# Optimization experiments

Hardware: AMD Instinct MI355X
Metric: run time of the kernel (lower is better)

Reference implementation:

```python
import jax, jax.numpy as jnp
import numpy as np

BS, L, K, SIM, CIN, COUT, HID = 8, 256, 5, 4, 32, 32, 64
LEXP = (SIM + 1) * (L - 1) + 1  # 1276


def setup_inputs() -> dict:
    key = jax.random.key(0)
    ks = jax.random.split(key, 6)
    # event timestamps: sorted within each sequence
    true_times = jnp.sort(jax.random.uniform(ks[0], (BS, L)) * 100.0, axis=-1)
    times = jnp.sort(jax.random.uniform(ks[1], (BS, LEXP)) * 100.0, axis=-1)
    true_features = jax.random.normal(ks[2], (BS, L, CIN))
    non_pad_mask = jnp.ones((BS, L), dtype=bool)
    # per-pair kernel MLP: (..., CIN) -> (..., CIN, COUT)
    W1 = jax.random.normal(ks[3], (CIN, HID)) * 0.1
    b1 = jnp.zeros((HID,))
    W2 = jax.random.normal(ks[4], (HID, CIN * COUT)) * 0.1
    b2 = jnp.zeros((CIN * COUT,))
    return dict(times=times, true_times=true_times, true_features=true_features,
                non_pad_mask=non_pad_mask, W1=W1, b1=b1, W2=W2, b2=b2, sim_size=SIM)


def _temporal_enc(dt, cin):
    # sin on even channels, cos on odd channels of dt / 10000^(2*(i//2)/cin)
    pos = jnp.asarray([10000.0 ** (2.0 * (i // 2) / cin) for i in range(cin)], dt.dtype)
    r = dt[..., None] / pos
    parity = jnp.arange(cin) % 2
    return jnp.where(parity == 0, jnp.sin(r), jnp.cos(r))


def reference(times, true_times, true_features, non_pad_mask, W1, b1, W2, b2, sim_size):
    bs, Lm = true_times.shape
    cin = true_features.shape[-1]
    # The torch identity-conv1d trick gathers, per output position t, the
    # kernel_size events at lags K..1 (t+j-K, j=0..K-1), zero-padded on the left.
    idx = jnp.arange(Lm)[None, :] + jnp.arange(K)[:, None]          # (K, L) indices into left-padded seq
    tt_pad = jnp.pad(true_times, ((0, 0), (K, 0)))
    pct = tt_pad[:, idx]                                            # (bs, K, L)
    tf_pad = jnp.pad(true_features, ((0, 0), (K, 0), (0, 0)))
    pcf = tf_pad[:, idx, :]                                         # (bs, K, L, cin)
    m_pad = jnp.pad(non_pad_mask, ((0, 0), (K, 0)))
    dt_mask = m_pad[:, idx] & non_pad_mask[:, None, :]              # (bs, K, L)

    s = int(sim_size)
    rep = s + 1
    # expand each true-time slot over the sim grid: Lexp = rep*(L-1)+1
    pct = jnp.repeat(pct, rep, axis=-1)
    pcf = jnp.repeat(pcf, rep, axis=2)
    dtm = jnp.repeat(dt_mask, rep, axis=-1)
    if s > 0:
        pct = pct[..., :-s]
        pcf = pcf[:, :, :-s, :]
    dtm = dtm[..., s:]                                              # mask shifted by sim_size (as in torch)

    delta = times[:, None, :] - pct                                 # (bs, K, Lexp)
    delta = jnp.where(dtm, delta, 0.0)
    pcf = jnp.where(dtm[..., None], pcf, 0.0)

    te = _temporal_enc(delta, cin)                                  # (bs, K, Lexp, cin)
    h = jax.nn.relu(te @ W1 + b1)
    kv = (h @ W2 + b2).reshape(*te.shape[:-1], cin, W2.shape[-1] // cin)  # (bs,K,Lexp,cin,cout)
    # torch also zeroes kv at ~dt_mask, but pcf is already zero there, so the
    # product (and its gradients) are identical without the redundant mask.
    out = jnp.einsum('bkli,bklio->blo', pcf, kv)                    # sum over K and cin
    return out
```

## Files before the change

### kernel.cpp

```cpp
#include <hip/hip_runtime.h>
#include <hip/hip_bf16.h>
#include <math.h>

#define BS   8
#define LL   256
#define KK   5
#define REP  5
#define LEXP 1276
#define TPB  40
#define NTILE (BS*TPB)
#define NF   12

typedef __attribute__((ext_vector_type(8)))  short bf16x8;
typedef __attribute__((ext_vector_type(16))) float f32x16;
typedef __attribute__((ext_vector_type(4)))  int   int4v;

__device__ __forceinline__ int pk_bf16(float lo, float hi) {
  __hip_bfloat162 v = __float22bfloat162_rn(make_float2(lo, hi));
  union { __hip_bfloat162 b; int i; } u; u.b = v; return u.i;
}
__device__ __forceinline__ bf16x8 to_bf(int4v v) {
  union { int4v i; bf16x8 b; } u; u.i = v; return u.b;
}

__device__ __constant__ const float IPC_TAB[16] = {
  0.15915494309189535f,   0.08950250709812862f,  0.050331651737107575f, 0.028302732511355427f,
  0.015915494309189534f,  0.008950250709812862f, 0.005033165173710758f, 0.002830273251135543f,
  0.0015915494309189536f, 0.0008950250709812862f,0.0005033165173710758f,0.0002830273251135543f,
  0.00015915494309189535f,8.950250709812862e-05f,5.033165173710758e-05f,2.830273251135543e-05f
};

__global__ __launch_bounds__(256) void k_w2f(
    const float* __restrict__ W2,
    int4v* __restrict__ W2F)
{
  const int u = blockIdx.x * 256 + threadIdx.x;
  const int nt = u >> 7, s = (u >> 6) & 1, lane = u & 63;
  const int col = lane & 31, hi = lane >> 5;
  const int np = nt * 32 + col, o = np >> 6, h = np & 63;
  const float* w2p = W2 + h * 1024 + o;
  int4v v;
  #pragma unroll
  for (int d = 0; d < 4; ++d) {
    const int i = s * 16 + hi * 8 + 2 * d;
    v[d] = pk_bf16(w2p[i * 32], w2p[(i + 1) * 32]);
  }
  W2F[u] = v;
}

__global__ __launch_bounds__(512) void k_fused(
    const float* __restrict__ times,
    const float* __restrict__ TT,
    const float* __restrict__ tf,
    const float* __restrict__ W1,
    const float* __restrict__ b1,
    const float* __restrict__ b2,
    const int4v* __restrict__ W2F,
    float* __restrict__ out)
{
  __shared__ unsigned short Al[NF][2048];
  __shared__ float Bcs[NF][32];

  const int t    = threadIdx.x;
  const int w    = t >> 6, lane = t & 63;
  const int col  = lane & 31, hi = lane >> 5;

  const int tile = blockIdx.x;
  const int b    = tile / TPB;
  const int j0   = (tile - b * TPB) * 32;
  const int jq_lo = j0 / REP;
  const int jtop  = (j0 + 31 < LEXP) ? (j0 + 31) : (LEXP - 1);
  const int jq_hi = jtop / REP;
  const int f_lo  = (jq_lo >= KK) ? (jq_lo - KK) : 0;
  const int f_hi  = jq_hi - 1;
  const int nf    = f_hi - f_lo + 1;

  bf16x8 tff[2];
  {
    const bool vf = col < nf;
    const float* tfp = tf + (size_t)(b * LL + f_lo + (vf ? col : 0)) * 32;
    #pragma unroll
    for (int s = 0; s < 2; ++s) {
      int4v v;
      #pragma unroll
      for (int d = 0; d < 4; ++d) {
        const int i = s * 16 + hi * 8 + 2 * d;
        v[d] = vf ? pk_bf16(tfp[i], tfp[i + 1]) : 0;
      }
      tff[s] = to_bf(v);
    }
  }

  #pragma unroll 2
  for (int nt = w; nt < 64; nt += 8) {
    const int4v a0 = W2F[(nt * 2 + 0) * 64 + lane];
    const int4v a1 = W2F[(nt * 2 + 1) * 64 + lane];
    f32x16 c = {};
    c = __builtin_amdgcn_mfma_f32_32x32x16_bf16(to_bf(a0), tff[0], c, 0, 0, 0);
    c = __builtin_amdgcn_mfma_f32_32x32x16_bf16(to_bf(a1), tff[1], c, 0, 0, 0);
    if (col < nf) {
      #pragma unroll
      for (int q = 0; q < 4; ++q) {
        const int u  = nt * 4 + q;
        const int up = u ^ ((u >> 3) & 7) ^ (col & 7);
        uint2 d2;
        d2.x = (unsigned)pk_bf16(c[4*q+0], c[4*q+1]);
        d2.y = (unsigned)pk_bf16(c[4*q+2], c[4*q+3]);
        *(uint2*)((char*)&Al[0][0] + col * 4096 + up * 16 + hi * 8) = d2;
      }
    }
  }

  if (t < NF * 32) {
    const int fl = t >> 5, o = t & 31;
    if (fl < nf) {
      const float* tfp = tf + (size_t)(b * LL + f_lo + fl) * 32;
      float acc = 0.0f;
      #pragma unroll
      for (int i = 0; i < 32; ++i) acc += tfp[i] * b2[i * 32 + o];
      Bcs[fl][o] = acc;
    }
  }

  int4v w1f[2][2];
  #pragma unroll
  for (int t2 = 0; t2 < 2; ++t2)
    #pragma unroll
    for (int ks = 0; ks < 2; ++ks) {
      const int h = t2 * 32 + col, c0 = ks * 16 + hi * 8;
      int4v v;
      v.x = pk_bf16(W1[(c0 + 0) * 64 + h], W1[(c0 + 1) * 64 + h]);
      v.y = pk_bf16(W1[(c0 + 2) * 64 + h], W1[(c0 + 3) * 64 + h]);
      v.z = pk_bf16(W1[(c0 + 4) * 64 + h], W1[(c0 + 5) * 64 + h]);
      v.w = pk_bf16(W1[(c0 + 6) * 64 + h], W1[(c0 + 7) * 64 + h]);
      w1f[t2][ks] = v;
    }
  f32x16 b1c0 = {}, b1c1 = {};
  #pragma unroll
  for (int gg = 0; gg < 16; ++gg) {
    const int rh = (gg & 3) + 8 * (gg >> 2) + 4 * hi;
    b1c0[gg] = b1[rh]; b1c1[gg] = b1[32 + rh];
  }
  float ipc[2][4];
  #pragma unroll
  for (int ks = 0; ks < 2; ++ks)
    #pragma unroll
    for (int d = 0; d < 4; ++d)
      ipc[ks][d] = IPC_TAB[hi * 4 + ks * 8 + d];

  const int j   = j0 + col;
  const bool vj = j < LEXP;
  const int jq  = (vj ? j : LEXP - 1) / REP;
  const float tj = times[b * LEXP + (vj ? j : LEXP - 1)];

  __syncthreads();

  f32x16 co = {};
  for (int fl = w; fl < nf; fl += 8) {
    const int f = f_lo + fl;
    int4v af[4];
    #pragma unroll
    for (int s = 0; s < 4; ++s) {
      const int u  = col * 8 + s * 2 + hi;
      const int up = u ^ ((u >> 3) & 7) ^ (fl & 7);
      af[s] = *(const int4v*)((const char*)&Al[0][0] + fl * 4096 + up * 16);
    }
    const float dt = tj - TT[b * LL + f];
    const int dd   = jq - f;
    const bool vm  = vj && (dd >= 1) && (dd <= KK);

    int4v te0, te1;
    {
      float r;
      r = dt * ipc[0][0]; te0.x = vm ? pk_bf16(__builtin_amdgcn_sinf(r), __builtin_amdgcn_cosf(r)) : 0;
      r = dt * ipc[0][1]; te0.y = vm ? pk_bf16(__builtin_amdgcn_sinf(r), __builtin_amdgcn_cosf(r)) : 0;
      r = dt * ipc[0][2]; te0.z = vm ? pk_bf16(__builtin_amdgcn_sinf(r), __builtin_amdgcn_cosf(r)) : 0;
      r = dt * ipc[0][3]; te0.w = vm ? pk_bf16(__builtin_amdgcn_sinf(r), __builtin_amdgcn_cosf(r)) : 0;
      r = dt * ipc[1][0]; te1.x = vm ? pk_bf16(__builtin_amdgcn_sinf(r), __builtin_amdgcn_cosf(r)) : 0;
      r = dt * ipc[1][1]; te1.y = vm ? pk_bf16(__builtin_amdgcn_sinf(r), __builtin_amdgcn_cosf(r)) : 0;
      r = dt * ipc[1][2]; te1.z = vm ? pk_bf16(__builtin_amdgcn_sinf(r), __builtin_amdgcn_cosf(r)) : 0;
      r = dt * ipc[1][3]; te1.w = vm ? pk_bf16(__builtin_amdgcn_sinf(r), __builtin_amdgcn_cosf(r)) : 0;
    }

    f32x16 h0 = __builtin_amdgcn_mfma_f32_32x32x16_bf16(to_bf(w1f[0][0]), to_bf(te0), b1c0, 0, 0, 0);
    h0 = __builtin_amdgcn_mfma_f32_32x32x16_bf16(to_bf(w1f[0][1]), to_bf(te1), h0, 0, 0, 0);
    f32x16 h1 = __builtin_amdgcn_mfma_f32_32x32x16_bf16(to_bf(w1f[1][0]), to_bf(te0), b1c1, 0, 0, 0);
    h1 = __builtin_amdgcn_mfma_f32_32x32x16_bf16(to_bf(w1f[1][1]), to_bf(te1), h1, 0, 0, 0);
    #pragma unroll
    for (int gg = 0; gg < 16; ++gg) { h0[gg] = fmaxf(h0[gg], 0.0f); h1[gg] = fmaxf(h1[gg], 0.0f); }

    #pragma unroll
    for (int s = 0; s < 4; ++s) {
      const int off = (s & 1) * 8;
      float e0,e1,e2,e3,e4,e5,e6,e7;
      if (s < 2) { e0=h0[off+0];e1=h0[off+1];e2=h0[off+2];e3=h0[off+3];e4=h0[off+4];e5=h0[off+5];e6=h0[off+6];e7=h0[off+7]; }
      else       { e0=h1[off+0];e1=h1[off+1];e2=h1[off+2];e3=h1[off+3];e4=h1[off+4];e5=h1[off+5];e6=h1[off+6];e7=h1[off+7]; }
      const int p0 = pk_bf16(e0, e1);
      const int p1 = pk_bf16(e2, e3);
      const int p2 = pk_bf16(e4, e5);
      const int p3 = pk_bf16(e6, e7);
      auto s0 = __builtin_amdgcn_permlane32_swap(p0, p2, false, false);
      auto s1 = __builtin_amdgcn_permlane32_swap(p1, p3, false, false);
      int4v hf; hf.x = s0[0]; hf.y = s1[0]; hf.z = s0[1]; hf.w = s1[1];
      co = __builtin_amdgcn_mfma_f32_32x32x16_bf16(to_bf(hf), to_bf(af[s]), co, 0, 0, 0);
    }
  }

  __syncthreads();
  float* part = (float*)&Al[0][0];
  if (w > 0) {
    #pragma unroll
    for (int gg = 0; gg < 16; ++gg) part[((w - 1) * 64 + lane) * 17 + gg] = co[gg];
  }
  __syncthreads();
  if (w == 0) {
    #pragma unroll
    for (int gg = 0; gg < 16; ++gg) {
      const int rl = (gg & 3) + 8 * (gg >> 2) + 4 * hi;
      const int jr = j0 + rl;
      if (jr < LEXP) {
        float v = co[gg];
        #pragma unroll
        for (int x = 0; x < 7; ++x) v += part[(x * 64 + lane) * 17 + gg];
        const int jqr = jr / REP;
        float sb = 0.0f;
        #pragma unroll
        for (int dd = 1; dd <= KK; ++dd) {
          const int fp = jqr - dd;
          if (fp >= 0) sb += Bcs[fp - f_lo][col];
        }
        out[((size_t)b * LEXP + jr) * 32 + col] = v + sb;
      }
    }
  }
}

extern "C" void kernel_launch(void* const* d_in, const int* in_sizes, int n_in,
                              void* d_out, int out_size, void* d_ws, size_t ws_size,
                              hipStream_t stream) {
  const float* times = (const float*)d_in[0];
  const float* TT    = (const float*)d_in[1];
  const float* tf    = (const float*)d_in[2];
  const float* W1    = (const float*)d_in[4];
  const float* b1    = (const float*)d_in[5];
  const float* W2    = (const float*)d_in[6];
  const float* b2    = (const float*)d_in[7];

  int4v* W2F = (int4v*)d_ws;

  k_w2f  <<<dim3(32),    dim3(256), 0, stream>>>(W2, W2F);
  k_fused<<<dim3(NTILE), dim3(512), 0, stream>>>(times, TT, tf, W1, b1, b2, W2F,
                                                 (float*)d_out);
}
```

Baseline: 31.10 us.

## Fold W2 prepack kernel into main kernel using fp32 FMA contraction

Removes the separate W2 bf16 repacking kernel launch and computes the per-feature contraction of W2 with true features directly inside the main kernel using scalar fp32 FMAs, reading W2 from global memory. True features are staged transposed in shared memory and reused for the b2 bias term as well. This saves a launch and the workspace round trip, but each block now re-reads all of W2 (256 KB fp32) and performs the contraction on vector ALUs instead of MFMA, adding per-block work and memory traffic.

```diff
diff --git a/kernel.cpp b/kernel.cpp
--- a/kernel.cpp
+++ b/kernel.cpp
@@ -30,35 +30,18 @@
   0.00015915494309189535f,8.950250709812862e-05f,5.033165173710758e-05f,2.830273251135543e-05f
 };
 
-__global__ __launch_bounds__(256) void k_w2f(
-    const float* __restrict__ W2,
-    int4v* __restrict__ W2F)
-{
-  const int u = blockIdx.x * 256 + threadIdx.x;
-  const int nt = u >> 7, s = (u >> 6) & 1, lane = u & 63;
-  const int col = lane & 31, hi = lane >> 5;
-  const int np = nt * 32 + col, o = np >> 6, h = np & 63;
-  const float* w2p = W2 + h * 1024 + o;
-  int4v v;
-  #pragma unroll
-  for (int d = 0; d < 4; ++d) {
-    const int i = s * 16 + hi * 8 + 2 * d;
-    v[d] = pk_bf16(w2p[i * 32], w2p[(i + 1) * 32]);
-  }
-  W2F[u] = v;
-}
-
-__global__ __launch_bounds__(512) void k_fused(
+__global__ __launch_bounds__(512) void k_all(
     const float* __restrict__ times,
     const float* __restrict__ TT,
     const float* __restrict__ tf,
     const float* __restrict__ W1,
     const float* __restrict__ b1,
+    const float* __restrict__ W2,
     const float* __restrict__ b2,
-    const int4v* __restrict__ W2F,
     float* __restrict__ out)
 {
-  __shared__ unsigned short Al[NF][2048];
+  __shared__ __align__(16) unsigned short Al[NF][2048];
+  __shared__ __align__(16) float tfsT[32][NF];
   __shared__ float Bcs[NF][32];
 
   const int t    = threadIdx.x;
@@ -75,38 +58,43 @@
   const int f_hi  = jq_hi - 1;
   const int nf    = f_hi - f_lo + 1;
 
-  bf16x8 tff[2];
+  if (t < NF * 32) {
+    const int fl = t >> 5, i = t & 31;
+    tfsT[i][fl] = (fl < nf) ? tf[(size_t)(b * LL + f_lo + fl) * 32 + i] : 0.0f;
+  }
+  __syncthreads();
+
+  const int h0 = (t >> 5) * 4;
+  float acc[NF][4] = {};
   {
-    const bool vf = col < nf;
-    const float* tfp = tf + (size_t)(b * LL + f_lo + (vf ? col : 0)) * 32;
-    #pragma unroll
-    for (int s = 0; s < 2; ++s) {
-      int4v v;
+    const float* w2p = W2 + h0 * 1024 + col;
+    #pragma unroll 8
+    for (int i = 0; i < 32; ++i) {
+      float wv[4];
       #pragma unroll
-      for (int d = 0; d < 4; ++d) {
-        const int i = s * 16 + hi * 8 + 2 * d;
-        v[d] = vf ? pk_bf16(tfp[i], tfp[i + 1]) : 0;
-      }
-      tff[s] = to_bf(v);
-    }
-  }
-
-  #pragma unroll 2
-  for (int nt = w; nt < 64; nt += 8) {
-    const int4v a0 = W2F[(nt * 2 + 0) * 64 + lane];
-    const int4v a1 = W2F[(nt * 2 + 1) * 64 + lane];
-    f32x16 c = {};
-    c = __builtin_amdgcn_mfma_f32_32x32x16_bf16(to_bf(a0), tff[0], c, 0, 0, 0);
-    c = __builtin_amdgcn_mfma_f32_32x32x16_bf16(to_bf(a1), tff[1], c, 0, 0, 0);
-    if (col < nf) {
+      for (int hs = 0; hs < 4; ++hs) wv[hs] = w2p[hs * 1024 + i * 32];
+      float tv[NF];
+      *(float4*)&tv[0] = *(const float4*)&tfsT[i][0];
+      *(float4*)&tv[4] = *(const float4*)&tfsT[i][4];
+      *(float4*)&tv[8] = *(const float4*)&tfsT[i][8];
       #pragma unroll
-      for (int q = 0; q < 4; ++q) {
-        const int u  = nt * 4 + q;
-        const int up = u ^ ((u >> 3) & 7) ^ (col & 7);
+      for (int fl = 0; fl < NF; ++fl)
+        #pragma unroll
+        for (int hs = 0; hs < 4; ++hs)
+          acc[fl][hs] = fmaf(wv[hs], tv[fl], acc[fl][hs]);
+    }
+  }
+  {
+    const int ubase = col * 8 + (h0 >> 3);
+    const int slot  = (h0 >> 1) & 3;
+    #pragma unroll
+    for (int fl = 0; fl < NF; ++fl) {
+      if (fl < nf) {
+        const int up = ubase ^ ((ubase >> 3) & 7) ^ (fl & 7);
         uint2 d2;
-        d2.x = (unsigned)pk_bf16(c[4*q+0], c[4*q+1]);
-        d2.y = (unsigned)pk_bf16(c[4*q+2], c[4*q+3]);
-        *(uint2*)((char*)&Al[0][0] + col * 4096 + up * 16 + hi * 8) = d2;
+        d2.x = (unsigned)pk_bf16(acc[fl][0], acc[fl][1]);
+        d2.y = (unsigned)pk_bf16(acc[fl][2], acc[fl][3]);
+        *(uint2*)((char*)&Al[0][0] + fl * 4096 + up * 16 + slot * 4) = d2;
       }
     }
   }
@@ -114,11 +102,10 @@
   if (t < NF * 32) {
     const int fl = t >> 5, o = t & 31;
     if (fl < nf) {
-      const float* tfp = tf + (size_t)(b * LL + f_lo + fl) * 32;
-      float acc = 0.0f;
+      float a2 = 0.0f;
       #pragma unroll
-      for (int i = 0; i < 32; ++i) acc += tfp[i] * b2[i * 32 + o];
-      Bcs[fl][o] = acc;
+      for (int i = 0; i < 32; ++i) a2 += tfsT[i][fl] * b2[i * 32 + o];
+      Bcs[fl][o] = a2;
     }
   }
 
@@ -182,19 +169,19 @@
       r = dt * ipc[1][3]; te1.w = vm ? pk_bf16(__builtin_amdgcn_sinf(r), __builtin_amdgcn_cosf(r)) : 0;
     }
 
-    f32x16 h0 = __builtin_amdgcn_mfma_f32_32x32x16_bf16(to_bf(w1f[0][0]), to_bf(te0), b1c0, 0, 0, 0);
-    h0 = __builtin_amdgcn_mfma_f32_32x32x16_bf16(to_bf(w1f[0][1]), to_bf(te1), h0, 0, 0, 0);
-    f32x16 h1 = __builtin_amdgcn_mfma_f32_32x32x16_bf16(to_bf(w1f[1][0]), to_bf(te0), b1c1, 0, 0, 0);
-    h1 = __builtin_amdgcn_mfma_f32_32x32x16_bf16(to_bf(w1f[1][1]), to_bf(te1), h1, 0, 0, 0);
-    #pragma unroll
-    for (int gg = 0; gg < 16; ++gg) { h0[gg] = fmaxf(h0[gg], 0.0f); h1[gg] = fmaxf(h1[gg], 0.0f); }
+    f32x16 h0v = __builtin_amdgcn_mfma_f32_32x32x16_bf16(to_bf(w1f[0][0]), to_bf(te0), b1c0, 0, 0, 0);
+    h0v = __builtin_amdgcn_mfma_f32_32x32x16_bf16(to_bf(w1f[0][1]), to_bf(te1), h0v, 0, 0, 0);
+    f32x16 h1v = __builtin_amdgcn_mfma_f32_32x32x16_bf16(to_bf(w1f[1][0]), to_bf(te0), b1c1, 0, 0, 0);
+    h1v = __builtin_amdgcn_mfma_f32_32x32x16_bf16(to_bf(w1f[1][1]), to_bf(te1), h1v, 0, 0, 0);
+    #pragma unroll
+    for (int gg = 0; gg < 16; ++gg) { h0v[gg] = fmaxf(h0v[gg], 0.0f); h1v[gg] = fmaxf(h1v[gg], 0.0f); }
 
     #pragma unroll
     for (int s = 0; s < 4; ++s) {
       const int off = (s & 1) * 8;
       float e0,e1,e2,e3,e4,e5,e6,e7;
-      if (s < 2) { e0=h0[off+0];e1=h0[off+1];e2=h0[off+2];e3=h0[off+3];e4=h0[off+4];e5=h0[off+5];e6=h0[off+6];e7=h0[off+7]; }
-      else       { e0=h1[off+0];e1=h1[off+1];e2=h1[off+2];e3=h1[off+3];e4=h1[off+4];e5=h1[off+5];e6=h1[off+6];e7=h1[off+7]; }
+      if (s < 2) { e0=h0v[off+0];e1=h0v[off+1];e2=h0v[off+2];e3=h0v[off+3];e4=h0v[off+4];e5=h0v[off+5];e6=h0v[off+6];e7=h0v[off+7]; }
+      else       { e0=h1v[off+0];e1=h1v[off+1];e2=h1v[off+2];e3=h1v[off+3];e4=h1v[off+4];e5=h1v[off+5];e6=h1v[off+6];e7=h1v[off+7]; }
       const int p0 = pk_bf16(e0, e1);
       const int p1 = pk_bf16(e2, e3);
       const int p2 = pk_bf16(e4, e5);
@@ -246,9 +233,6 @@
   const float* W2    = (const float*)d_in[6];
   const float* b2    = (const float*)d_in[7];
 
-  int4v* W2F = (int4v*)d_ws;
-
-  k_w2f  <<<dim3(32),    dim3(256), 0, stream>>>(W2, W2F);
-  k_fused<<<dim3(NTILE), dim3(512), 0, stream>>>(times, TT, tf, W1, b1, b2, W2F,
-                                                 (float*)d_out);
-}
+  k_all<<<dim3(NTILE), dim3(512), 0, stream>>>(times, TT, tf, W1, b1, W2, b2,
+                                               (float*)d_out);
+}
```

Result: faster. 29.42 us (-5.4%).
